# Optimization experiments

Measured on AMD Instinct MI355X. Metric: run time of the kernel, lower is better.

Reference implementation:

```python
import jax, jax.numpy as jnp
import numpy as np

EMB = 64
NEG = 0.2  # DGL GATConv default negative_slope

def seg_sum(x, ids, n):
    return jax.ops.segment_sum(x, ids, num_segments=n)

def seg_max(x, ids, n):
    return jax.ops.segment_max(x, ids, num_segments=n)

def gat(x, src, dst, W, al, ar):
    # DGL GATConv: fc (no bias), per-head additive attention, edge softmax over in-edges of dst
    N = x.shape[0]
    H, D = al.shape
    h = (x @ W).reshape(N, H, D)                 # (N,H,D)
    el = jnp.sum(h * al, -1)                     # (N,H)
    er = jnp.sum(h * ar, -1)                     # (N,H)
    e = jax.nn.leaky_relu(el[src] + er[dst], negative_slope=NEG)  # (E,H)
    m = seg_max(e, dst, N)
    ex = jnp.exp(e - m[dst])
    den = seg_sum(ex, dst, N)
    alpha = ex / den[dst]                        # (E,H)
    return seg_sum(alpha[..., None] * h[src], dst, N)  # (N,H,D)

def conv1d(x, w, b):
    y = jax.lax.conv_general_dilated(x, w, (1,), 'VALID', dimension_numbers=('NCH', 'OIH', 'NCH'))
    return y + b[None, :, None]

def maxpool1d(x, k, s):
    return jax.lax.reduce_window(x, -jnp.inf, jax.lax.max, (1, 1, k), (1, 1, s), 'VALID')

def textcnn(pad_dmap, c1w, c1b, c2w, c2b, c3w, c3b):
    x = jnp.squeeze(pad_dmap, 1).transpose(0, 2, 1)   # (B, emb, L)
    x = maxpool1d(conv1d(x, c1w, c1b), 3, 3)
    x = maxpool1d(conv1d(x, c2w, c2b), 3, 3)
    x = maxpool1d(conv1d(x, c3w, c3b), 130, 1)        # (B,128,1)
    return jnp.squeeze(x, 2)

def branch(feat, src, dst, nid, pad_dmap, ng, p):
    g = jax.nn.relu(gat(feat, src, dst, p['Wg1'], p['al1'], p['ar1'])).reshape(-1, EMB * 3)
    g = jax.nn.relu(gat(g, src, dst, p['Wg2'], p['al2'], p['ar2'])).reshape(-1, EMB * 9)
    g = jax.nn.relu(gat(g, src, dst, p['Wg3'], p['al3'], p['ar3'])).reshape(-1, EMB * 9)
    gmax = seg_max(g, nid, ng)                        # graph-level MaxPooling readout
    g = jax.nn.relu(gmax @ p['fcg_w'] + p['fcg_b'])
    s = textcnn(pad_dmap, p['c1w'], p['c1b'], p['c2w'], p['c2b'], p['c3w'], p['c3b'])
    s = jax.nn.relu(s @ p['tf_w'] + p['tf_b'])
    w = jax.nn.sigmoid(p['w1'])
    return (1.0 - w) * g + w * s

PKEYS = ['Wg1', 'al1', 'ar1', 'Wg2', 'al2', 'ar2', 'Wg3', 'al3', 'ar3', 'fcg_w', 'fcg_b',
         'c1w', 'c1b', 'c2w', 'c2b', 'c3w', 'c3b', 'tf_w', 'tf_b', 'w1',
         'fc1_w', 'fc1_b', 'fc2_w', 'fc2_b', 'out_w', 'out_b']

def forward(feat1, feat2, pad_dmap1, pad_dmap2, params, src1, dst1, src2, dst2, nid1, nid2, num_graphs):
    p = dict(zip(PKEYS, params))
    gc1 = branch(feat1, src1, dst1, nid1, pad_dmap1, num_graphs, p)
    gc2 = branch(feat2, src2, dst2, nid2, pad_dmap2, num_graphs, p)
    gc = jnp.concatenate([gc1, gc2], axis=1)
    gc = jax.nn.relu(gc @ p['fc1_w'] + p['fc1_b'])   # dropout is identity at eval
    gc = jax.nn.relu(gc @ p['fc2_w'] + p['fc2_b'])
    return jax.nn.sigmoid(gc @ p['out_w'] + p['out_b'])

def setup_inputs() -> dict:
    key = jax.random.key(0)
    ks = jax.random.split(key, 40)
    N, E, B, L = 8000, 160000, 16, 1200
    d = {}
    d['feat1'] = jax.random.normal(ks[0], (N, EMB), jnp.float32)
    d['feat2'] = jax.random.normal(ks[1], (N, EMB), jnp.float32)
    d['pad_dmap1'] = jax.random.normal(ks[2], (B, 1, L, EMB), jnp.float32)
    d['pad_dmap2'] = jax.random.normal(ks[3], (B, 1, L, EMB), jnp.float32)
    d['src1'] = jax.random.randint(ks[4], (E,), 0, N, jnp.int32)
    d['dst1'] = jax.random.randint(ks[5], (E,), 0, N, jnp.int32)
    d['src2'] = jax.random.randint(ks[6], (E,), 0, N, jnp.int32)
    d['dst2'] = jax.random.randint(ks[7], (E,), 0, N, jnp.int32)
    nid = ((jnp.arange(N) * B) // N).astype(jnp.int32)  # sorted, all graphs non-empty
    d['nid1'] = nid
    d['nid2'] = nid
    d['num_graphs'] = B
    def lin(k, i, o):
        return jax.random.normal(k, (i, o), jnp.float32) * np.float32(1.0 / np.sqrt(i))
    d['Wg1'] = lin(ks[8], EMB, EMB * 3)
    d['al1'] = jax.random.normal(ks[9], (3, EMB), jnp.float32) * 0.1
    d['ar1'] = jax.random.normal(ks[10], (3, EMB), jnp.float32) * 0.1
    d['Wg2'] = lin(ks[11], EMB * 3, EMB * 9)
    d['al2'] = jax.random.normal(ks[12], (3, EMB * 3), jnp.float32) * 0.1
    d['ar2'] = jax.random.normal(ks[13], (3, EMB * 3), jnp.float32) * 0.1
    d['Wg3'] = lin(ks[14], EMB * 9, EMB * 9)
    d['al3'] = jax.random.normal(ks[15], (1, EMB * 9), jnp.float32) * 0.1
    d['ar3'] = jax.random.normal(ks[16], (1, EMB * 9), jnp.float32) * 0.1
    d['fcg_w'] = lin(ks[17], EMB * 9, 128)
    d['fcg_b'] = jnp.zeros((128,), jnp.float32)
    d['c1w'] = jax.random.normal(ks[18], (128, EMB, 3), jnp.float32) * np.float32(1.0 / np.sqrt(EMB * 3))
    d['c1b'] = jnp.zeros((128,), jnp.float32)
    d['c2w'] = jax.random.normal(ks[19], (128, 128, 3), jnp.float32) * np.float32(1.0 / np.sqrt(128 * 3))
    d['c2b'] = jnp.zeros((128,), jnp.float32)
    d['c3w'] = jax.random.normal(ks[20], (128, 128, 3), jnp.float32) * np.float32(1.0 / np.sqrt(128 * 3))
    d['c3b'] = jnp.zeros((128,), jnp.float32)
    d['tf_w'] = lin(ks[21], 128, 128)
    d['tf_b'] = jnp.zeros((128,), jnp.float32)
    d['w1'] = jnp.full((1,), 0.5, jnp.float32)
    d['fc1_w'] = lin(ks[22], 256, 512)
    d['fc1_b'] = jnp.zeros((512,), jnp.float32)
    d['fc2_w'] = lin(ks[23], 512, 256)
    d['fc2_b'] = jnp.zeros((256,), jnp.float32)
    d['out_w'] = lin(ks[24], 256, 1)
    d['out_b'] = jnp.zeros((1,), jnp.float32)
    return d

def reference(feat1, src1, dst1, nid1, pad_dmap1, feat2, src2, dst2, nid2, pad_dmap2, num_graphs,
              Wg1, al1, ar1, Wg2, al2, ar2, Wg3, al3, ar3, fcg_w, fcg_b,
              c1w, c1b, c2w, c2b, c3w, c3b, tf_w, tf_b, w1,
              fc1_w, fc1_b, fc2_w, fc2_b, out_w, out_b):
    params = (Wg1, al1, ar1, Wg2, al2, ar2, Wg3, al3, ar3, fcg_w, fcg_b,
              c1w, c1b, c2w, c2b, c3w, c3b, tf_w, tf_b, w1,
              fc1_w, fc1_b, fc2_w, fc2_b, out_w, out_b)
    return forward(feat1, feat2, pad_dmap1, pad_dmap2, params, src1, dst1, src2, dst2, nid1, nid2, num_graphs)
```

## Files before the change

### kernel.cpp

```cpp
#include <hip/hip_runtime.h>
#include <hip/hip_bf16.h>
#include <math.h>

#define NEG_SLOPE 0.2f

__global__ void zero_i32(int* __restrict__ p, int n) {
    int i = blockIdx.x * blockDim.x + threadIdx.x;
    if (i < n) p[i] = 0;
}

__global__ void count_edges2(const int* __restrict__ dst0, const int* __restrict__ dst1,
                             int* __restrict__ cnt, int N, int E) {
    int i = blockIdx.x * blockDim.x + threadIdx.x;
    if (i >= 2 * E) return;
    int br = i >= E;
    int j = i - br * E;
    const int* d = br ? dst1 : dst0;
    atomicAdd(&cnt[br * N + d[j]], 1);
}

__global__ void scan_block(int* __restrict__ cnt_all, int* __restrict__ rs_all, int N) {
    __shared__ int s[1024];
    int br = blockIdx.x;
    int* cnt = cnt_all + br * N;
    int* rs = rs_all + br * (N + 1);
    int tid = threadIdx.x;
    int running = 0;
    for (int base = 0; base < N; base += 1024) {
        int v = (base + tid < N) ? cnt[base + tid] : 0;
        if (base + tid < N) cnt[base + tid] = 0;
        __syncthreads();
        s[tid] = v;
        __syncthreads();
        for (int off = 1; off < 1024; off <<= 1) {
            int t = (tid >= off) ? s[tid - off] : 0;
            __syncthreads();
            if (tid >= off) s[tid] += t;
            __syncthreads();
        }
        if (base + tid < N) rs[base + tid] = running + s[tid] - v;
        running += s[1023];
    }
    if (tid == 0) rs[N] = running;
}

__global__ void scatter_edges2(const int* __restrict__ dst0, const int* __restrict__ dst1,
                               const int* __restrict__ rs_all, int* __restrict__ fill_all,
                               int* __restrict__ eidx_all, int N, int E) {
    int i = blockIdx.x * blockDim.x + threadIdx.x;
    if (i >= 2 * E) return;
    int br = i >= E;
    int j = i - br * E;
    const int* d = br ? dst1 : dst0;
    int dd = d[j];
    int pos = atomicAdd(&fill_all[br * N + dd], 1);
    eidx_all[br * E + rs_all[br * (N + 1) + dd] + pos] = j;
}

__device__ __forceinline__ short f2bf(float x) {
    __hip_bfloat16 h = __float2bfloat16(x);
    return *reinterpret_cast<short*>(&h);
}
__device__ __forceinline__ float bf2f(short s) {
    unsigned int u = ((unsigned int)(unsigned short)s) << 16;
    return __uint_as_float(u);
}
__device__ __forceinline__ float us2f(unsigned short s) {
    return __uint_as_float((unsigned int)s << 16);
}

__device__ __forceinline__ void split_w_elem(const float* W, short* W2t, int K, int N, int idx) {
    int k = idx / N, n = idx - k * N;
    float x = W[idx];
    short hs = f2bf(x);
    short ls = f2bf(x - bf2f(hs));
    size_t base = (size_t)n * 2 * K;
    W2t[base + k] = hs;
    W2t[base + K + k] = ls;
}
__device__ __forceinline__ void split_cw_elem(const float* w, short* w2, int Kp, int idx) {
    int o = idx / Kp, k = idx - o * Kp;
    float x = w[idx];
    short hs = f2bf(x);
    short ls = f2bf(x - bf2f(hs));
    size_t base = (size_t)o * 2 * Kp;
    w2[base + k] = hs;
    w2[base + Kp + k] = ls;
}
__global__ void prep_weights(const float* __restrict__ Wg1, const float* __restrict__ Wg2,
                             const float* __restrict__ Wg3, const float* __restrict__ c1w,
                             const float* __restrict__ c2w, const float* __restrict__ c3w,
                             short* __restrict__ w2t1, short* __restrict__ w2t2,
                             short* __restrict__ w2t3, short* __restrict__ cw1,
                             short* __restrict__ cw2, short* __restrict__ cw3) {
    int idx = blockIdx.x * blockDim.x + threadIdx.x;
    if (idx < 12288)       split_w_elem(Wg1, w2t1, 64, 192, idx);
    else if (idx < 122880) split_w_elem(Wg2, w2t2, 192, 576, idx - 12288);
    else if (idx < 454656) split_w_elem(Wg3, w2t3, 576, 576, idx - 122880);
    else if (idx < 479232) split_cw_elem(c1w, cw1, 192, idx - 454656);
    else if (idx < 528384) split_cw_elem(c2w, cw2, 384, idx - 479232);
    else if (idx < 577536) split_cw_elem(c3w, cw3, 384, idx - 528384);
}

typedef __attribute__((ext_vector_type(8))) short short8;
typedef __attribute__((ext_vector_type(4))) short short4v;
typedef __attribute__((ext_vector_type(4))) float floatx4;

__global__ __launch_bounds__(256) void gemm_bf3_v4(const float* __restrict__ A0,
                                                   const float* __restrict__ A1,
                                                   const short* __restrict__ Bt,
                                                   unsigned short* __restrict__ Cbf,
                                                   int M, int K, int N, size_t cBrStride) {
    __shared__ __align__(16) short sA[64 * 72];
    __shared__ __align__(16) short sB[192 * 72];
    int tid = threadIdx.x;
    int wave = tid >> 6, lane = tid & 63;
    int m = lane & 15, q = lane >> 4;
    int row0 = blockIdx.y << 6;
    int col0 = blockIdx.x * 192;
    const float* A = blockIdx.z ? A1 : A0;
    unsigned short* Cbfb = Cbf + blockIdx.z * cBrStride;
    int K2 = K * 2;
    floatx4 acc[4][3];
#pragma unroll
    for (int rt = 0; rt < 4; ++rt)
#pragma unroll
        for (int ct = 0; ct < 3; ++ct) acc[rt][ct] = (floatx4){0.f, 0.f, 0.f, 0.f};

    for (int k0 = 0; k0 < K; k0 += 32) {
#pragma unroll
        for (int p = 0; p < 2; ++p) {
            int t = tid + (p << 8);
            int r = t >> 3, c = (t & 7) << 2;
            float4 av = *(const float4*)&A[(size_t)(row0 + r) * K + k0 + c];
            short4v hs, ls;
            hs[0] = f2bf(av.x); ls[0] = f2bf(av.x - bf2f(hs[0]));
            hs[1] = f2bf(av.y); ls[1] = f2bf(av.y - bf2f(hs[1]));
            hs[2] = f2bf(av.z); ls[2] = f2bf(av.z - bf2f(hs[2]));
            hs[3] = f2bf(av.w); ls[3] = f2bf(av.w - bf2f(hs[3]));
            *(short4v*)&sA[r * 72 + c] = hs;
            *(short4v*)&sA[r * 72 + 32 + c] = ls;
        }
#pragma unroll
        for (int p = 0; p < 6; ++p) {
            int t = tid + (p << 8);
            int n = t >> 3, sub = t & 7;
            int srcoff = k0 + (sub << 3) + ((sub >= 4) ? (K - 32) : 0);
            *(float4*)&sB[n * 72 + (sub << 3)] =
                *(const float4*)&Bt[(size_t)(col0 + n) * K2 + srcoff];
        }
        __syncthreads();
        short8 a_hi[4], a_lo[4];
#pragma unroll
        for (int rt = 0; rt < 4; ++rt) {
            a_hi[rt] = *(const short8*)&sA[(rt * 16 + m) * 72 + q * 8];
            a_lo[rt] = *(const short8*)&sA[(rt * 16 + m) * 72 + 32 + q * 8];
        }
#pragma unroll
        for (int ct = 0; ct < 3; ++ct) {
            short8 b_hi = *(const short8*)&sB[(wave * 48 + ct * 16 + m) * 72 + q * 8];
            short8 b_lo = *(const short8*)&sB[(wave * 48 + ct * 16 + m) * 72 + 32 + q * 8];
#pragma unroll
            for (int rt = 0; rt < 4; ++rt) {
                acc[rt][ct] = __builtin_amdgcn_mfma_f32_16x16x32_bf16(a_hi[rt], b_hi, acc[rt][ct], 0, 0, 0);
                acc[rt][ct] = __builtin_amdgcn_mfma_f32_16x16x32_bf16(a_lo[rt], b_hi, acc[rt][ct], 0, 0, 0);
                acc[rt][ct] = __builtin_amdgcn_mfma_f32_16x16x32_bf16(a_hi[rt], b_lo, acc[rt][ct], 0, 0, 0);
            }
        }
        __syncthreads();
    }
#pragma unroll
    for (int rt = 0; rt < 4; ++rt)
#pragma unroll
        for (int ct = 0; ct < 3; ++ct)
#pragma unroll
            for (int r = 0; r < 4; ++r) {
                size_t idx = (size_t)(row0 + rt * 16 + q * 4 + r) * N + col0 + wave * 48 + ct * 16 + m;
                Cbfb[idx] = (unsigned short)f2bf(acc[rt][ct][r]);
            }
}

__global__ void gat_elr(const unsigned short* __restrict__ h, const float* __restrict__ al,
                        const float* __restrict__ ar, float* __restrict__ el,
                        float* __restrict__ er, int N, int H, int D,
                        size_t hBr, size_t eBr) {
    int wid = (blockIdx.x * blockDim.x + threadIdx.x) >> 6;
    int lane = threadIdx.x & 63;
    if (wid >= 2 * N * H) return;
    int br = wid / (N * H);
    int loc = wid - br * N * H;
    int n = loc / H, hh = loc - n * H;
    const unsigned short* hp = h + br * hBr + ((size_t)n * H + hh) * D;
    const float* alp = al + (size_t)hh * D;
    const float* arp = ar + (size_t)hh * D;
    float sl = 0.f, sr = 0.f;
    for (int d = lane; d < D; d += 64) {
        float v = us2f(hp[d]);
        sl += v * alp[d];
        sr += v * arp[d];
    }
    for (int off = 32; off > 0; off >>= 1) {
        sl += __shfl_down(sl, off, 64);
        sr += __shfl_down(sr, off, 64);
    }
    if (lane == 0) { el[br * eBr + loc] = sl; er[br * eBr + loc] = sr; }
}

__device__ __forceinline__ float lrelu(float v) {
    return (v > 0.f) ? v : NEG_SLOPE * v;
}

#define TILE_E 64
__global__ void gat_softagg(const unsigned short* __restrict__ hb_all,
                            const float* __restrict__ el_all, const float* __restrict__ er_all,
                            const int* __restrict__ src0, const int* __restrict__ src1,
                            const int* __restrict__ rs_all, const int* __restrict__ eidx_all,
                            float4* __restrict__ out4_all, int N, int H, int D, int E,
                            size_t hBr, size_t eBr, size_t o4Br) {
    __shared__ int s_src[TILE_E];
    __shared__ float s_alpha[TILE_E * 3];
    __shared__ float s_stat[6];
    int n = blockIdx.x;
    int br = blockIdx.y;
    const int* src = br ? src1 : src0;
    const int* rs = rs_all + br * (N + 1);
    const int* eidx = eidx_all + br * E;
    const unsigned short* hb = hb_all + br * hBr;
    const float* el = el_all + br * eBr;
    const float* er = er_all + br * eBr;
    float4* out4 = out4_all + br * o4Br;
    int HD = H * D;
    int HD4 = HD >> 2;
    int tid = threadIdx.x;
    int s0 = rs[n], s1 = rs[n + 1];
    int deg = s1 - s0;
    bool activeC = tid < HD4;
    int hh = activeC ? (tid << 2) / D : 0;
    float4 accA = {0.f, 0.f, 0.f, 0.f};
    float4 accB = {0.f, 0.f, 0.f, 0.f};

    if (deg > 0 && deg <= 64) {
        if (tid < 64) {
            int lane = tid;
            float ern0 = er[n * H + 0];
            float ern1 = (H > 1) ? er[n * H + 1] : 0.f;
            float ern2 = (H > 2) ? er[n * H + 2] : 0.f;
            int s = 0;
            float v0 = -INFINITY, v1 = -INFINITY, v2 = -INFINITY;
            if (lane < deg) {
                int e = eidx[s0 + lane];
                s = src[e];
                v0 = lrelu(el[s * H + 0] + ern0);
                if (H > 1) {
                    v1 = lrelu(el[s * H + 1] + ern1);
                    v2 = lrelu(el[s * H + 2] + ern2);
                }
            }
            float m0 = v0, m1 = v1, m2 = v2;
#pragma unroll
            for (int off = 32; off > 0; off >>= 1) {
                m0 = fmaxf(m0, __shfl_xor(m0, off, 64));
                m1 = fmaxf(m1, __shfl_xor(m1, off, 64));
                m2 = fmaxf(m2, __shfl_xor(m2, off, 64));
            }
            float ex0 = (lane < deg) ? expf(v0 - m0) : 0.f;
            float ex1 = (lane < deg && H > 1) ? expf(v1 - m1) : 0.f;
            float ex2 = (lane < deg && H > 2) ? expf(v2 - m2) : 0.f;
            float d0 = ex0, d1 = ex1, d2 = ex2;
#pragma unroll
            for (int off = 32; off > 0; off >>= 1) {
                d0 += __shfl_xor(d0, off, 64);
                d1 += __shfl_xor(d1, off, 64);
                d2 += __shfl_xor(d2, off, 64);
            }
            if (lane < deg) {
                s_src[lane] = s;
                s_alpha[lane * 3 + 0] = ex0 / d0;
                if (H > 1) {
                    s_alpha[lane * 3 + 1] = ex1 / d1;
                    s_alpha[lane * 3 + 2] = ex2 / d2;
                }
            }
        }
        __syncthreads();
        if (activeC) {
            int i = 0;
#pragma unroll 4
            for (; i + 1 < deg; i += 2) {
                float a0 = s_alpha[i * 3 + hh];
                float a1 = s_alpha[(i + 1) * 3 + hh];
                ushort4 h0 = *(const ushort4*)&hb[(size_t)s_src[i] * HD + (tid << 2)];
                ushort4 h1 = *(const ushort4*)&hb[(size_t)s_src[i + 1] * HD + (tid << 2)];
                accA.x += a0 * us2f(h0.x); accA.y += a0 * us2f(h0.y);
                accA.z += a0 * us2f(h0.z); accA.w += a0 * us2f(h0.w);
                accB.x += a1 * us2f(h1.x); accB.y += a1 * us2f(h1.y);
                accB.z += a1 * us2f(h1.z); accB.w += a1 * us2f(h1.w);
            }
            if (i < deg) {
                float a0 = s_alpha[i * 3 + hh];
                ushort4 h0 = *(const ushort4*)&hb[(size_t)s_src[i] * HD + (tid << 2)];
                accA.x += a0 * us2f(h0.x); accA.y += a0 * us2f(h0.y);
                accA.z += a0 * us2f(h0.z); accA.w += a0 * us2f(h0.w);
            }
        }
    } else if (deg > 64) {
        if (tid < 64) {
            int lane = tid;
            float ern0 = er[n * H + 0];
            float ern1 = (H > 1) ? er[n * H + 1] : 0.f;
            float ern2 = (H > 2) ? er[n * H + 2] : 0.f;
            float m0 = -INFINITY, m1 = -INFINITY, m2 = -INFINITY;
            for (int j = s0 + lane; j < s1; j += 64) {
                int e = eidx[j], s = src[e];
                m0 = fmaxf(m0, lrelu(el[s * H + 0] + ern0));
                if (H > 1) {
                    m1 = fmaxf(m1, lrelu(el[s * H + 1] + ern1));
                    m2 = fmaxf(m2, lrelu(el[s * H + 2] + ern2));
                }
            }
#pragma unroll
            for (int off = 32; off > 0; off >>= 1) {
                m0 = fmaxf(m0, __shfl_xor(m0, off, 64));
                m1 = fmaxf(m1, __shfl_xor(m1, off, 64));
                m2 = fmaxf(m2, __shfl_xor(m2, off, 64));
            }
            float d0 = 0.f, d1 = 0.f, d2 = 0.f;
            for (int j = s0 + lane; j < s1; j += 64) {
                int e = eidx[j], s = src[e];
                d0 += expf(lrelu(el[s * H + 0] + ern0) - m0);
                if (H > 1) {
                    d1 += expf(lrelu(el[s * H + 1] + ern1) - m1);
                    d2 += expf(lrelu(el[s * H + 2] + ern2) - m2);
                }
            }
#pragma unroll
            for (int off = 32; off > 0; off >>= 1) {
                d0 += __shfl_xor(d0, off, 64);
                d1 += __shfl_xor(d1, off, 64);
                d2 += __shfl_xor(d2, off, 64);
            }
            if (lane == 0) {
                s_stat[0] = m0; s_stat[1] = m1; s_stat[2] = m2;
                s_stat[3] = 1.f / d0;
                s_stat[4] = (H > 1) ? 1.f / d1 : 0.f;
                s_stat[5] = (H > 2) ? 1.f / d2 : 0.f;
            }
        }
        __syncthreads();
        float m0 = s_stat[0], m1 = s_stat[1], m2 = s_stat[2];
        float i0 = s_stat[3], i1 = s_stat[4], i2 = s_stat[5];
        for (int base = s0; base < s1; base += TILE_E) {
            int cnt = s1 - base; if (cnt > TILE_E) cnt = TILE_E;
            __syncthreads();
            if (tid < cnt) {
                int e = eidx[base + tid], s = src[e];
                s_src[tid] = s;
                s_alpha[tid * 3 + 0] = expf(lrelu(el[s * H + 0] + er[n * H + 0]) - m0) * i0;
                if (H > 1) {
                    s_alpha[tid * 3 + 1] = expf(lrelu(el[s * H + 1] + er[n * H + 1]) - m1) * i1;
                    s_alpha[tid * 3 + 2] = expf(lrelu(el[s * H + 2] + er[n * H + 2]) - m2) * i2;
                }
            }
            __syncthreads();
            if (activeC) {
                int i = 0;
#pragma unroll 2
                for (; i + 1 < cnt; i += 2) {
                    float a0 = s_alpha[i * 3 + hh];
                    float a1 = s_alpha[(i + 1) * 3 + hh];
                    ushort4 h0 = *(const ushort4*)&hb[(size_t)s_src[i] * HD + (tid << 2)];
                    ushort4 h1 = *(const ushort4*)&hb[(size_t)s_src[i + 1] * HD + (tid << 2)];
                    accA.x += a0 * us2f(h0.x); accA.y += a0 * us2f(h0.y);
                    accA.z += a0 * us2f(h0.z); accA.w += a0 * us2f(h0.w);
                    accB.x += a1 * us2f(h1.x); accB.y += a1 * us2f(h1.y);
                    accB.z += a1 * us2f(h1.z); accB.w += a1 * us2f(h1.w);
                }
                if (i < cnt) {
                    float a0 = s_alpha[i * 3 + hh];
                    ushort4 h0 = *(const ushort4*)&hb[(size_t)s_src[i] * HD + (tid << 2)];
                    accA.x += a0 * us2f(h0.x); accA.y += a0 * us2f(h0.y);
                    accA.z += a0 * us2f(h0.z); accA.w += a0 * us2f(h0.w);
                }
            }
        }
    }
    if (activeC) {
        float4 acc;
        acc.x = fmaxf(accA.x + accB.x, 0.f);
        acc.y = fmaxf(accA.y + accB.y, 0.f);
        acc.z = fmaxf(accA.z + accB.z, 0.f);
        acc.w = fmaxf(accA.w + accB.w, 0.f);
        out4[(size_t)n * HD4 + tid] = acc;
    }
}

__global__ void seg_max_atomic(const float* __restrict__ g_all, const int* __restrict__ nid,
                               int* __restrict__ out_all, int N, int C,
                               size_t gBr, size_t oBr) {
    int br = blockIdx.y;
    const float* g = g_all + br * gBr;
    int* out = out_all + br * oBr;
    int n0 = blockIdx.x << 5;
    int n1 = n0 + 32; if (n1 > N) n1 = N;
    if (n0 >= N) return;
    for (int c = threadIdx.x; c < C; c += blockDim.x) {
        int cur = nid[n0];
        float m = 0.f;
        for (int n = n0; n < n1; ++n) {
            int gid = nid[n];
            if (gid != cur) {
                atomicMax(&out[cur * C + c], __float_as_int(m));
                cur = gid; m = 0.f;
            }
            m = fmaxf(m, g[(size_t)n * C + c]);
        }
        atomicMax(&out[cur * C + c], __float_as_int(m));
    }
}

__global__ void linear_wave(const float* __restrict__ in, const float* __restrict__ W,
                            const float* __restrict__ bias, float* __restrict__ out,
                            int K, int O, int act, size_t inBr, size_t outBr) {
    int o = blockIdx.x * 4 + (threadIdx.x >> 6);
    int b = blockIdx.y;
    int lane = threadIdx.x & 63;
    if (o >= O) return;
    const float* ip = in + blockIdx.z * inBr + (size_t)b * K;
    float acc = 0.f;
    for (int k = lane; k < K; k += 64)
        acc += ip[k] * W[(size_t)k * O + o];
    for (int off = 32; off > 0; off >>= 1)
        acc += __shfl_down(acc, off, 64);
    if (lane == 0) {
        acc += bias[o];
        if (act == 1) acc = fmaxf(acc, 0.f);
        else if (act == 2) acc = 1.f / (1.f + expf(-acc));
        out[blockIdx.z * outBr + (size_t)b * O + o] = acc;
    }
}

__global__ void linear_cat(const float* __restrict__ gvec, const float* __restrict__ sf,
                           const float* __restrict__ w1, const float* __restrict__ W,
                           const float* __restrict__ bias, float* __restrict__ out,
                           int O, int B128) {
    int o = blockIdx.x * 4 + (threadIdx.x >> 6);
    int b = blockIdx.y;
    int lane = threadIdx.x & 63;
    if (o >= 512) return;
    float w = 1.f / (1.f + expf(-w1[0]));
    float acc = 0.f;
    for (int k = lane; k < 256; k += 64) {
        int br = k >> 7, c = k & 127;
        float v = (1.f - w) * gvec[br * B128 + b * 128 + c] + w * sf[br * B128 + b * 128 + c];
        acc += v * W[(size_t)k * 512 + o];
    }
    for (int off = 32; off > 0; off >>= 1)
        acc += __shfl_down(acc, off, 64);
    if (lane == 0)
        out[(size_t)b * 512 + o] = fmaxf(acc + bias[o], 0.f);
    (void)O;
}

__global__ __launch_bounds__(256) void conv_mfma(const float* __restrict__ x,
                                                 const float* __restrict__ x1,
                                                 const short* __restrict__ w2,
                                                 const float* __restrict__ bias,
                                                 float* __restrict__ y,
                                                 int Cin, int Lin, int Lout,
                                                 int mode, int srcLen,
                                                 size_t xBr, size_t yBr) {
    extern __shared__ __align__(16) char smem[];
    float* sx = (float*)smem;
    short* sB = (short*)(smem + (size_t)Cin * 68 * 4);
    int Kp = Cin * 3;
    int K2 = Kp * 2;
    int b = blockIdx.y;
    float* yb = y + blockIdx.z * yBr + (size_t)b * 128 * Lout;
    int l0 = blockIdx.x << 6;
    int tid = threadIdx.x;
    int wave = tid >> 6, lane = tid & 63;
    int m = lane & 15, q = lane >> 4;
    int wrow = (wave & 1) << 5;
    int wcol = (wave >> 1) << 6;
    int loadL = Lin - l0; if (loadL > 66) loadL = 66;
    if (mode == 2) {
        const float* pb = (blockIdx.z ? x1 : x) + (size_t)b * 1200 * 64;
        for (int t = tid; t < loadL * 64; t += 256) {
            int i = t >> 6, c = t & 63;
            sx[c * 68 + i] = pb[(size_t)(l0 + i) * 64 + c];
        }
    } else if (mode == 1) {
        const float* xb = x + blockIdx.z * xBr + (size_t)b * Cin * srcLen;
        for (int t = tid; t < Cin * loadL; t += 256) {
            int c = t / loadL, i = t - c * loadL;
            const float* row = &xb[(size_t)c * srcLen + 3 * (l0 + i)];
            sx[c * 68 + i] = fmaxf(fmaxf(row[0], row[1]), row[2]);
        }
    } else {
        const float* xb = x + blockIdx.z * xBr + (size_t)b * Cin * srcLen;
        for (int t = tid; t < Cin * loadL; t += 256) {
            int c = t / loadL, i = t - c * loadL;
            sx[c * 68 + i] = xb[(size_t)c * srcLen + l0 + i];
        }
    }
    floatx4 acc[2][4];
#pragma unroll
    for (int rt = 0; rt < 2; ++rt)
#pragma unroll
        for (int ct = 0; ct < 4; ++ct) acc[rt][ct] = (floatx4){0.f, 0.f, 0.f, 0.f};

    for (int k0 = 0; k0 < Kp; k0 += 32) {
#pragma unroll
        for (int p = 0; p < 4; ++p) {
            int t = tid + (p << 8);
            int o = t >> 3, slot = t & 7;
            int srcoff = k0 + ((slot & 3) << 3) + ((slot >= 4) ? Kp : 0);
            *(float4*)&sB[o * 72 + (slot << 3)] = *(const float4*)&w2[(size_t)o * K2 + srcoff];
        }
        __syncthreads();
        short8 a_hi[2], a_lo[2];
#pragma unroll
        for (int rt = 0; rt < 2; ++rt) {
            int pos = wrow + rt * 16 + m;
#pragma unroll
            for (int kk = 0; kk < 8; ++kk) {
                int k = k0 + q * 8 + kk;
                int c = k / 3, j = k - c * 3;
                float v = sx[c * 68 + pos + j];
                short hv = f2bf(v);
                a_hi[rt][kk] = hv;
                a_lo[rt][kk] = f2bf(v - bf2f(hv));
            }
        }
#pragma unroll
        for (int ct = 0; ct < 4; ++ct) {
            short8 b_hi = *(const short8*)&sB[(wcol + ct * 16 + m) * 72 + q * 8];
            short8 b_lo = *(const short8*)&sB[(wcol + ct * 16 + m) * 72 + 32 + q * 8];
#pragma unroll
            for (int rt = 0; rt < 2; ++rt) {
                acc[rt][ct] = __builtin_amdgcn_mfma_f32_16x16x32_bf16(a_hi[rt], b_hi, acc[rt][ct], 0, 0, 0);
                acc[rt][ct] = __builtin_amdgcn_mfma_f32_16x16x32_bf16(a_lo[rt], b_hi, acc[rt][ct], 0, 0, 0);
                acc[rt][ct] = __builtin_amdgcn_mfma_f32_16x16x32_bf16(a_hi[rt], b_lo, acc[rt][ct], 0, 0, 0);
            }
        }
        __syncthreads();
    }
#pragma unroll
    for (int ct = 0; ct < 4; ++ct) {
        int o = wcol + ct * 16 + m;
        float bv = bias[o];
#pragma unroll
        for (int rt = 0; rt < 2; ++rt)
#pragma unroll
            for (int r = 0; r < 4; ++r) {
                int pos = wrow + rt * 16 + q * 4 + r;
                if (l0 + pos < Lout)
                    yb[(size_t)o * Lout + l0 + pos] = acc[rt][ct][r] + bv;
            }
    }
}

__global__ void pooltf(const float* __restrict__ y3, const float* __restrict__ tf_w,
                       const float* __restrict__ tf_b, float* __restrict__ sf,
                       size_t yBr, size_t sfBr) {
    __shared__ float s_sp[128];
    int b = blockIdx.x, br = blockIdx.y;
    const float* yb = y3 + br * yBr + (size_t)b * 128 * 130;
    int c = threadIdx.x;
    float mx = -INFINITY;
    for (int l = 0; l < 130; ++l) mx = fmaxf(mx, yb[(size_t)c * 130 + l]);
    s_sp[c] = mx;
    __syncthreads();
    int o = threadIdx.x;
    float acc = tf_b[o];
    for (int k = 0; k < 128; ++k) acc += s_sp[k] * tf_w[(size_t)k * 128 + o];
    sf[br * sfBr + (size_t)b * 128 + o] = fmaxf(acc, 0.f);
}

extern "C" void kernel_launch(void* const* d_in, const int* in_sizes, int n_in,
                              void* d_out, int out_size, void* d_ws, size_t ws_size,
                              hipStream_t stream) {
    const float* feat[2] = {(const float*)d_in[0], (const float*)d_in[1]};
    const float* pad[2]  = {(const float*)d_in[2], (const float*)d_in[3]};
    const int* src[2]    = {(const int*)d_in[4], (const int*)d_in[6]};
    const int* dst[2]    = {(const int*)d_in[5], (const int*)d_in[7]};
    const int* nid[2]    = {(const int*)d_in[8], (const int*)d_in[9]};
    const float* Wg[3]   = {(const float*)d_in[11], (const float*)d_in[14], (const float*)d_in[17]};
    const float* al[3]   = {(const float*)d_in[12], (const float*)d_in[15], (const float*)d_in[18]};
    const float* ar[3]   = {(const float*)d_in[13], (const float*)d_in[16], (const float*)d_in[19]};
    const float* fcg_w = (const float*)d_in[20]; const float* fcg_b = (const float*)d_in[21];
    const float* c1w = (const float*)d_in[22];   const float* c1b = (const float*)d_in[23];
    const float* c2w = (const float*)d_in[24];   const float* c2b = (const float*)d_in[25];
    const float* c3w = (const float*)d_in[26];   const float* c3b = (const float*)d_in[27];
    const float* tf_w = (const float*)d_in[28];  const float* tf_b = (const float*)d_in[29];
    const float* w1 = (const float*)d_in[30];
    const float* fc1_w = (const float*)d_in[31]; const float* fc1_b = (const float*)d_in[32];
    const float* fc2_w = (const float*)d_in[33]; const float* fc2_b = (const float*)d_in[34];
    const float* outw = (const float*)d_in[35];  const float* outb = (const float*)d_in[36];
    float* out = (float*)d_out;

    const int N = in_sizes[0] / 64;
    const int E = in_sizes[4];
    const int B = 16, L = 1200;
    const size_t NS = (size_t)N * 576;

    char* wsb = (char*)d_ws;
    size_t off = 0;
    auto allocB = [&](size_t bytes) -> void* {
        void* p = wsb + off;
        off += (bytes + 255) & ~(size_t)255;
        return p;
    };
    auto alloc = [&](size_t elems) -> void* { return allocB(elems * 4); };

    unsigned short* h_bf = (unsigned short*)allocB(2 * NS * 2);
    float* gA    = (float*)alloc(2 * NS);
    float* el    = (float*)alloc(2 * (size_t)N * 3);
    float* er    = (float*)alloc(2 * (size_t)N * 3);
    int* rs      = (int*)alloc(2 * (N + 1));
    int* cnt     = (int*)alloc(2 * N);
    int* eidx    = (int*)alloc(2 * E);
    int* gmax    = (int*)alloc(2 * (size_t)B * 576);
    float* gvec  = (float*)alloc(2 * (size_t)B * 128);
    float* sf    = (float*)alloc(2 * (size_t)B * 128);
    float* f1    = (float*)alloc((size_t)B * 512);
    float* f2    = (float*)alloc((size_t)B * 256);
    short* w2t1  = (short*)allocB((size_t)192 * 2 * 64 * 2);
    short* w2t2  = (short*)allocB((size_t)576 * 2 * 192 * 2);
    short* w2t3  = (short*)allocB((size_t)576 * 2 * 576 * 2);
    short* cw1   = (short*)allocB((size_t)128 * 2 * 192 * 2);
    short* cw2   = (short*)allocB((size_t)128 * 2 * 384 * 2);
    short* cw3   = (short*)allocB((size_t)128 * 2 * 384 * 2);
    size_t tcnn_elems = 2 * (size_t)B * 128 * (1198 + 397 + 130);
    size_t uni_elems = 2 * NS > tcnn_elems ? 2 * NS : tcnn_elems;
    float* uni = (float*)alloc(uni_elems);
    float* gB = uni;
    float* y1 = uni;
    float* y2 = y1 + 2 * (size_t)B * 128 * 1198;
    float* y3 = y2 + 2 * (size_t)B * 128 * 397;
    (void)ws_size; (void)n_in; (void)out_size;

    prep_weights<<<2256, 256, 0, stream>>>(Wg[0], Wg[1], Wg[2], c1w, c2w, c3w,
                                           w2t1, w2t2, w2t3, cw1, cw2, cw3);
    short* w2t[3] = {w2t1, w2t2, w2t3};

    zero_i32<<<(2 * N + 255) / 256, 256, 0, stream>>>(cnt, 2 * N);
    count_edges2<<<(2 * E + 255) / 256, 256, 0, stream>>>(dst[0], dst[1], cnt, N, E);
    scan_block<<<2, 1024, 0, stream>>>(cnt, rs, N);
    scatter_edges2<<<(2 * E + 255) / 256, 256, 0, stream>>>(dst[0], dst[1], rs, cnt, eidx, N, E);

    const int dims[3][3] = {{64, 3, 64}, {192, 3, 192}, {576, 1, 576}};
    float* outs[3] = {gA, gB, gA};
    const float* inp0 = feat[0];
    const float* inp1 = feat[1];
    for (int ly = 0; ly < 3; ++ly) {
        int K = dims[ly][0], H = dims[ly][1], D = dims[ly][2];
        int HD = H * D;
        gemm_bf3_v4<<<dim3(HD / 192, N / 64, 2), 256, 0, stream>>>(inp0, inp1, w2t[ly], h_bf,
                                                                   N, K, HD, NS);
        int waves2 = 2 * N * H;
        gat_elr<<<((size_t)waves2 * 64 + 255) / 256, 256, 0, stream>>>(h_bf, al[ly], ar[ly], el, er,
                                                                       N, H, D, NS, (size_t)N * 3);
        int aggThreads = (((HD >> 2) + 63) / 64) * 64;
        gat_softagg<<<dim3(N, 2), aggThreads, 0, stream>>>(
            h_bf, el, er, src[0], src[1], rs, eidx, (float4*)outs[ly],
            N, H, D, E, NS, (size_t)N * 3, NS / 4);
        inp0 = outs[ly];
        inp1 = outs[ly] + NS;
    }
    zero_i32<<<(2 * B * 576 + 255) / 256, 256, 0, stream>>>(gmax, 2 * B * 576);
    seg_max_atomic<<<dim3((N + 31) / 32, 2), 256, 0, stream>>>(gA, nid[0], gmax, N, 576,
                                                               NS, (size_t)B * 576);
    linear_wave<<<dim3(32, B, 2), 256, 0, stream>>>((const float*)gmax, fcg_w, fcg_b, gvec,
                                                    576, 128, 1, (size_t)B * 576, (size_t)B * 128);

    conv_mfma<<<dim3(19, B, 2), 256, 64 * 68 * 4 + 128 * 72 * 2, stream>>>(
        pad[0], pad[1], cw1, c1b, y1, 64, 1200, 1198, 2, 0,
        0, (size_t)B * 128 * 1198);
    conv_mfma<<<dim3(7, B, 2), 256, 128 * 68 * 4 + 128 * 72 * 2, stream>>>(
        y1, nullptr, cw2, c2b, y2, 128, 399, 397, 1, 1198,
        (size_t)B * 128 * 1198, (size_t)B * 128 * 397);
    conv_mfma<<<dim3(3, B, 2), 256, 128 * 68 * 4 + 128 * 72 * 2, stream>>>(
        y2, nullptr, cw3, c3b, y3, 128, 132, 130, 1, 397,
        (size_t)B * 128 * 397, (size_t)B * 128 * 130);
    pooltf<<<dim3(B, 2), 128, 0, stream>>>(y3, tf_w, tf_b, sf,
                                           (size_t)B * 128 * 130, (size_t)B * 128);

    linear_cat<<<dim3(128, B, 1), 256, 0, stream>>>(gvec, sf, w1, fc1_w, fc1_b, f1, 512, B * 128);
    linear_wave<<<dim3(64, B, 1), 256, 0, stream>>>(f1, fc2_w, fc2_b, f2, 512, 256, 1, 0, 0);
    linear_wave<<<dim3(1, B, 1), 256, 0, stream>>>(f2, outw, outb, out, 256, 1, 2, 0, 0);
}
```

Before: 557.1 us.

## Fuse head MLP into one kernel and merge zeroing launches

The three head layers (fc1, fc2 and output sigmoid) now run in one kernel with one block per batch row. Intermediates stay in shared memory, which removes two launches and the global round-trips for f1 and f2. The two zeroing kernels are also merged into a single launch. The cost is less parallelism in the head: each block does a serial 256- or 512-long dot product per thread instead of wave-wide reductions over many blocks.

```diff
diff --git a/kernel.cpp b/kernel.cpp
--- a/kernel.cpp
+++ b/kernel.cpp
@@ -4,9 +4,10 @@
 
 #define NEG_SLOPE 0.2f
 
-__global__ void zero_i32(int* __restrict__ p, int n) {
+__global__ void zero2_i32(int* __restrict__ a, int na, int* __restrict__ b, int nb) {
     int i = blockIdx.x * blockDim.x + threadIdx.x;
-    if (i < n) p[i] = 0;
+    if (i < na) a[i] = 0;
+    else if (i < na + nb) b[i - na] = 0;
 }
 
 __global__ void count_edges2(const int* __restrict__ dst0, const int* __restrict__ dst1,
@@ -439,26 +440,44 @@
     }
 }
 
-__global__ void linear_cat(const float* __restrict__ gvec, const float* __restrict__ sf,
-                           const float* __restrict__ w1, const float* __restrict__ W,
-                           const float* __restrict__ bias, float* __restrict__ out,
-                           int O, int B128) {
-    int o = blockIdx.x * 4 + (threadIdx.x >> 6);
-    int b = blockIdx.y;
-    int lane = threadIdx.x & 63;
-    if (o >= 512) return;
+__global__ __launch_bounds__(256) void head_mlp(
+        const float* __restrict__ gvec, const float* __restrict__ sf,
+        const float* __restrict__ w1, const float* __restrict__ fc1_w,
+        const float* __restrict__ fc1_b, const float* __restrict__ fc2_w,
+        const float* __restrict__ fc2_b, const float* __restrict__ outw,
+        const float* __restrict__ outb, float* __restrict__ out, int B128) {
+    __shared__ float s_v[256];
+    __shared__ float s_f1[512];
+    __shared__ float s_f2[256];
+    __shared__ float s_r[4];
+    int b = blockIdx.x;
+    int t = threadIdx.x;
     float w = 1.f / (1.f + expf(-w1[0]));
-    float acc = 0.f;
-    for (int k = lane; k < 256; k += 64) {
-        int br = k >> 7, c = k & 127;
-        float v = (1.f - w) * gvec[br * B128 + b * 128 + c] + w * sf[br * B128 + b * 128 + c];
-        acc += v * W[(size_t)k * 512 + o];
-    }
-    for (int off = 32; off > 0; off >>= 1)
-        acc += __shfl_down(acc, off, 64);
-    if (lane == 0)
-        out[(size_t)b * 512 + o] = fmaxf(acc + bias[o], 0.f);
-    (void)O;
+    {
+        int br = t >> 7, c = t & 127;
+        s_v[t] = (1.f - w) * gvec[br * B128 + b * 128 + c] + w * sf[br * B128 + b * 128 + c];
+    }
+    __syncthreads();
+    for (int o = t; o < 512; o += 256) {
+        float acc = fc1_b[o];
+        for (int k = 0; k < 256; ++k) acc += s_v[k] * fc1_w[(size_t)k * 512 + o];
+        s_f1[o] = fmaxf(acc, 0.f);
+    }
+    __syncthreads();
+    {
+        float acc = fc2_b[t];
+        for (int k = 0; k < 512; ++k) acc += s_f1[k] * fc2_w[(size_t)k * 256 + t];
+        s_f2[t] = fmaxf(acc, 0.f);
+    }
+    __syncthreads();
+    float p = s_f2[t] * outw[t];
+    for (int off = 32; off > 0; off >>= 1) p += __shfl_down(p, off, 64);
+    if ((t & 63) == 0) s_r[t >> 6] = p;
+    __syncthreads();
+    if (t == 0) {
+        float acc = s_r[0] + s_r[1] + s_r[2] + s_r[3] + outb[0];
+        out[b] = 1.f / (1.f + expf(-acc));
+    }
 }
 
 __global__ __launch_bounds__(256) void conv_mfma(const float* __restrict__ x,
@@ -623,8 +642,6 @@
     int* gmax    = (int*)alloc(2 * (size_t)B * 576);
     float* gvec  = (float*)alloc(2 * (size_t)B * 128);
     float* sf    = (float*)alloc(2 * (size_t)B * 128);
-    float* f1    = (float*)alloc((size_t)B * 512);
-    float* f2    = (float*)alloc((size_t)B * 256);
     short* w2t1  = (short*)allocB((size_t)192 * 2 * 64 * 2);
     short* w2t2  = (short*)allocB((size_t)576 * 2 * 192 * 2);
     short* w2t3  = (short*)allocB((size_t)576 * 2 * 576 * 2);
@@ -644,7 +661,7 @@
                                            w2t1, w2t2, w2t3, cw1, cw2, cw3);
     short* w2t[3] = {w2t1, w2t2, w2t3};
 
-    zero_i32<<<(2 * N + 255) / 256, 256, 0, stream>>>(cnt, 2 * N);
+    zero2_i32<<<(2 * N + 2 * B * 576 + 255) / 256, 256, 0, stream>>>(cnt, 2 * N, gmax, 2 * B * 576);
     count_edges2<<<(2 * E + 255) / 256, 256, 0, stream>>>(dst[0], dst[1], cnt, N, E);
     scan_block<<<2, 1024, 0, stream>>>(cnt, rs, N);
     scatter_edges2<<<(2 * E + 255) / 256, 256, 0, stream>>>(dst[0], dst[1], rs, cnt, eidx, N, E);
@@ -668,7 +685,6 @@
         inp0 = outs[ly];
         inp1 = outs[ly] + NS;
     }
-    zero_i32<<<(2 * B * 576 + 255) / 256, 256, 0, stream>>>(gmax, 2 * B * 576);
     seg_max_atomic<<<dim3((N + 31) / 32, 2), 256, 0, stream>>>(gA, nid[0], gmax, N, 576,
                                                                NS, (size_t)B * 576);
     linear_wave<<<dim3(32, B, 2), 256, 0, stream>>>((const float*)gmax, fcg_w, fcg_b, gvec,
@@ -686,7 +702,6 @@
     pooltf<<<dim3(B, 2), 128, 0, stream>>>(y3, tf_w, tf_b, sf,
                                            (size_t)B * 128 * 130, (size_t)B * 128);
 
-    linear_cat<<<dim3(128, B, 1), 256, 0, stream>>>(gvec, sf, w1, fc1_w, fc1_b, f1, 512, B * 128);
-    linear_wave<<<dim3(64, B, 1), 256, 0, stream>>>(f1, fc2_w, fc2_b, f2, 512, 256, 1, 0, 0);
-    linear_wave<<<dim3(1, B, 1), 256, 0, stream>>>(f2, outw, outb, out, 256, 1, 2, 0, 0);
-}
+    head_mlp<<<B, 256, 0, stream>>>(gvec, sf, w1, fc1_w, fc1_b, fc2_w, fc2_b,
+                                    outw, outb, out, B * 128);
+}
```

Measured after the change: 571.1 us. 1.03x slower.
